# Kernel optimization log

Hardware: AMD Instinct MI355X
Metric: run time of the kernel (lower is better)

The kernel has to match this reference:

```python
import math
import jax, jax.numpy as jnp
import numpy as np

D_MODEL, N_HEADS, QKV, D_HEAD, D_FF, N_BLOCKS, IN_DIM = 288, 8, 328, 41, 1315, 4, 83
B, S = 1024, 128
EPS = 1e-5


def setup_inputs() -> dict:
    key = jax.random.key(0)
    ks = iter(jax.random.split(key, 64))
    def rn(shape, scale=0.05):
        return jax.random.normal(next(ks), shape, jnp.float32) * scale
    inp = {
        "x": jax.random.normal(next(ks), (B, S, IN_DIM), jnp.float32),
        "Wp": rn((D_MODEL, IN_DIM)), "bp": rn((D_MODEL,)),
        "phase": rn((D_MODEL,)),
        "Wq": rn((N_BLOCKS, QKV, D_MODEL)), "bq": rn((N_BLOCKS, QKV)),
        "Wk": rn((N_BLOCKS, QKV, D_MODEL)), "bk": rn((N_BLOCKS, QKV)),
        "Wv": rn((N_BLOCKS, QKV, D_MODEL)), "bv": rn((N_BLOCKS, QKV)),
        "Wo": rn((N_BLOCKS, D_MODEL, QKV)), "bo": rn((N_BLOCKS, D_MODEL)),
        "temp": jnp.ones((N_BLOCKS,), jnp.float32) + rn((N_BLOCKS,), 0.01),
        "qscale": jnp.ones((N_BLOCKS, N_HEADS), jnp.float32) + rn((N_BLOCKS, N_HEADS), 0.01),
        "Wf1": rn((N_BLOCKS, D_FF, D_MODEL)), "bf1": rn((N_BLOCKS, D_FF)),
        "Wf2": rn((N_BLOCKS, D_MODEL, D_FF)), "bf2": rn((N_BLOCKS, D_MODEL)),
        "n1w": jnp.ones((N_BLOCKS, D_MODEL), jnp.float32), "n1b": jnp.zeros((N_BLOCKS, D_MODEL), jnp.float32),
        "n2w": jnp.ones((N_BLOCKS, D_MODEL), jnp.float32), "n2b": jnp.zeros((N_BLOCKS, D_MODEL), jnp.float32),
        "skip": jnp.ones((N_BLOCKS,), jnp.float32),
        "bn_w": jnp.ones((D_MODEL,), jnp.float32), "bn_b": jnp.zeros((D_MODEL,), jnp.float32),
        "bn_mean": rn((D_MODEL,)), "bn_var": jax.random.uniform(next(ks), (D_MODEL,), jnp.float32, 0.5, 1.5),
        "h1w": rn((144, D_MODEL)), "h1b": rn((144,)),
        "h2w": rn((72, 144)), "h2b": rn((72,)),
        "h3w": rn((1, 72)), "h3b": rn((1,)),
        "u1w": rn((72, D_MODEL)), "u1b": rn((72,)),
        "u2w": rn((1, 72)), "u2b": rn((1,)),
    }
    return inp


def _layer_norm(x, w, b):
    mu = jnp.mean(x, axis=-1, keepdims=True)
    var = jnp.mean((x - mu) ** 2, axis=-1, keepdims=True)
    return (x - mu) * jax.lax.rsqrt(var + EPS) * w + b


def reference(x, Wp, bp, phase, Wq, bq, Wk, bk, Wv, bv, Wo, bo, temp, qscale,
              Wf1, bf1, Wf2, bf2, n1w, n1b, n2w, n2b, skip,
              bn_w, bn_b, bn_mean, bn_var,
              h1w, h1b, h2w, h2b, h3w, h3b, u1w, u1b, u2w, u2b):
    Bsz, Sl, _ = x.shape
    # input projection
    h = jnp.einsum('bsi,di->bsd', x, Wp) + bp
    # sinusoidal positional encoding modulated by cos(quantum_phase)
    pos = jnp.arange(Sl, dtype=jnp.float32)[:, None]
    div = jnp.exp(jnp.arange(0, D_MODEL, 2, dtype=jnp.float32) * (-math.log(10000.0) / D_MODEL))
    pe = jnp.zeros((Sl, D_MODEL), jnp.float32)
    pe = pe.at[:, 0::2].set(jnp.sin(pos * div)).at[:, 1::2].set(jnp.cos(pos * div))
    h = h + pe * jnp.cos(phase)

    for l in range(N_BLOCKS):
        # attention with temperature-scaled softmax + post-softmax per-head scale
        q = (jnp.einsum('bsd,qd->bsq', h, Wq[l]) + bq[l]).reshape(Bsz, Sl, N_HEADS, D_HEAD)
        k = (jnp.einsum('bsd,qd->bsq', h, Wk[l]) + bk[l]).reshape(Bsz, Sl, N_HEADS, D_HEAD)
        v = (jnp.einsum('bsd,qd->bsq', h, Wv[l]) + bv[l]).reshape(Bsz, Sl, N_HEADS, D_HEAD)
        scale = math.sqrt(D_HEAD) * temp[l]
        scores = jnp.einsum('bqhd,bkhd->bhqk', q, k) / scale  # [B,H,S,S]
        attn = jax.nn.softmax(scores, axis=-1) * qscale[l][None, :, None, None]
        o = jnp.einsum('bhqk,bkhd->bqhd', attn, v).reshape(Bsz, Sl, QKV)
        o = jnp.einsum('bsq,dq->bsd', o, Wo[l]) + bo[l]
        h = _layer_norm(h + skip[l] * o, n1w[l], n1b[l])
        # GELU FFN (exact erf gelu, dropout inactive in eval)
        f = jax.nn.gelu(jnp.einsum('bsd,fd->bsf', h, Wf1[l]) + bf1[l], approximate=False)
        f = jnp.einsum('bsf,df->bsd', f, Wf2[l]) + bf2[l]
        h = _layer_norm(h + f, n2w[l], n2b[l])

    pooled = jnp.mean(h, axis=1)  # [B, D_MODEL]
    # output head: BatchNorm1d (eval, running stats) -> GELU -> MLP
    z = (pooled - bn_mean) * jax.lax.rsqrt(bn_var + EPS) * bn_w + bn_b
    z = jax.nn.gelu(z, approximate=False)
    z = jax.nn.gelu(z @ h1w.T + h1b, approximate=False)
    z = jax.nn.gelu(z @ h2w.T + h2b, approximate=False)
    pred = z @ h3w.T + h3b  # [B, 1]
    # uncertainty head
    u = jax.nn.relu(pooled @ u1w.T + u1b)
    unc = jax.nn.softplus(u @ u2w.T + u2b)  # [B, 1]
    return pred, unc
```

## Files before the change

kernel.cpp:

```cpp
#include <hip/hip_runtime.h>
#include <cstdint>

typedef __attribute__((ext_vector_type(8))) short short8;
typedef __attribute__((ext_vector_type(4))) short s4v;
typedef __attribute__((ext_vector_type(4))) float floatx4;

#define DEV __device__ __forceinline__

DEV short f2bf(float f) {
  unsigned u = __builtin_bit_cast(unsigned, f);
  u += 0x7fffu + ((u >> 16) & 1u);
  return (short)(u >> 16);
}
DEV short f2bf_ru(float f) {
  unsigned u = __builtin_bit_cast(unsigned, f);
  return (short)((u + 0x8000u) >> 16);
}
DEV float bf2f(short s) {
  unsigned u = ((unsigned)(unsigned short)s) << 16;
  return __builtin_bit_cast(float, u);
}
DEV float gelu_exact(float x) {
  return 0.5f * x * (1.0f + erff(x * 0.70710678118654752f));
}
DEV float gelu_fast(float x) {
  const float t2 = 1.5957691216057308f * (x + 0.044715f * x * x * x);
  return x / (1.0f + __expf(-t2));
}
DEV void gload16(const void* g, void* l) {
  __builtin_amdgcn_global_load_lds((const __attribute__((address_space(1))) void*)g,
                                   (__attribute__((address_space(3))) void*)l,
                                   16, 0, 0);
}

template<int MODE>
__global__ __launch_bounds__(256)
void gemm_kernel(const short* __restrict__ A, const short* __restrict__ Bw,
                 const float* __restrict__ bias, short* __restrict__ C,
                 const float* __restrict__ pe,
                 int K, int lda, int ldb, int ldc, int Nstore, int NT, long hstride)
{
  __shared__ __align__(16) short lds[128 * 136];
  short* Ct = lds;

  const int tid  = threadIdx.x;
  const int wave = tid >> 6, lane = tid & 63;
  const int quad = lane >> 4, r16 = lane & 15;
  const int per = gridDim.x >> 3;
  const int gti = (blockIdx.x & 7) * per + (blockIdx.x >> 3);
  const int mt = gti / NT, nt = gti - mt * NT;
  const int wm = (wave >> 1) * 64, wn = (wave & 1) * 64;

  const long Abase = (long)mt * 128 * lda;
  const long Bbase = (long)nt * 128 * ldb;

  const int row0 = tid >> 2,         cc0 = (tid & 3) ^ ((row0 >> 1) & 3);
  const int row1 = (256 + tid) >> 2, cc1 = ((256 + tid) & 3) ^ ((row1 >> 1) & 3);

  floatx4 acc[4][4] = {};

  auto stage = [&](short* As_, short* Bs_, int k0) {
    gload16(A  + Abase + (long)row0 * lda + k0 + cc0 * 8, &As_[(wave * 64) * 8]);
    gload16(A  + Abase + (long)row1 * lda + k0 + cc1 * 8, &As_[(256 + wave * 64) * 8]);
    gload16(Bw + Bbase + (long)row0 * ldb + k0 + cc0 * 8, &Bs_[(wave * 64) * 8]);
    gload16(Bw + Bbase + (long)row1 * ldb + k0 + cc1 * 8, &Bs_[(256 + wave * 64) * 8]);
  };
  auto compute = [&](const short* As_, const short* Bs_) {
    short8 af[4], bfr[4];
#pragma unroll
    for (int i = 0; i < 4; ++i) {
      const int R = wm + i * 16 + r16;
      af[i] = *(const short8*)&As_[R * 32 + (quad ^ ((R >> 1) & 3)) * 8];
    }
#pragma unroll
    for (int j = 0; j < 4; ++j) {
      const int R = wn + j * 16 + r16;
      bfr[j] = *(const short8*)&Bs_[R * 32 + (quad ^ ((R >> 1) & 3)) * 8];
    }
#pragma unroll
    for (int i = 0; i < 4; ++i)
#pragma unroll
      for (int j = 0; j < 4; ++j)
        acc[i][j] = __builtin_amdgcn_mfma_f32_16x16x32_bf16(bfr[j], af[i], acc[i][j], 0, 0, 0);
  };

  short* const A0  = lds;
  short* const Bb0 = lds + 4096;
  short* const A1  = lds + 8192;
  short* const Bb1 = lds + 12288;

  stage(A0, Bb0, 0);
  __syncthreads();
  int k0 = 0;
  while (true) {
    if (k0 + 32 < K) stage(A1, Bb1, k0 + 32);
    compute(A0, Bb0);
    __syncthreads();
    k0 += 32;
    if (k0 >= K) break;
    if (k0 + 32 < K) stage(A0, Bb0, k0 + 32);
    compute(A1, Bb1);
    __syncthreads();
    k0 += 32;
    if (k0 >= K) break;
  }

  const int mb0 = mt * 128, tb = nt * 128;

#pragma unroll
  for (int j = 0; j < 4; ++j) {
    const int n0 = wn + j * 16 + quad * 4;
    const floatx4 b4 = *(const floatx4*)&bias[tb + n0];
#pragma unroll
    for (int i = 0; i < 4; ++i) {
      const int m = wm + i * 16 + r16;
      floatx4 v = acc[i][j] + b4;
      if (MODE == 1) {
#pragma unroll
        for (int rg = 0; rg < 4; ++rg) v[rg] = gelu_fast(v[rg]);
      }
      if (MODE == 2) {
        const floatx4 p4 = *(const floatx4*)&pe[((mb0 + m) & 127) * 384 + tb + n0];
        v = v + p4;
      }
      s4v o4;
#pragma unroll
      for (int rg = 0; rg < 4; ++rg) o4[rg] = f2bf_ru(v[rg]);
      *(s4v*)&Ct[m * 136 + n0] = o4;
    }
  }
  __syncthreads();

#pragma unroll
  for (int rr = 0; rr < 8; ++rr) {
    const int chunk = rr * 256 + tid;
    const int row = chunk >> 4, ch = chunk & 15;
    const int gcol = tb + ch * 8;
    if (MODE == 3) {
      const int g = gcol / 48, d0 = gcol - g * 48;
      *(short8*)(C + (long)g * hstride + (long)(mb0 + row) * 48 + d0) =
          *(const short8*)&Ct[row * 136 + ch * 8];
    } else if (gcol < Nstore) {
      *(short8*)(C + (long)(mb0 + row) * ldc + gcol) = *(const short8*)&Ct[row * 136 + ch * 8];
    }
  }
}

template<bool AHEAD>
__global__ __launch_bounds__(512, 4)
void gemm_ln_kernel(const short* __restrict__ A, const short* __restrict__ Bw,
                    const float* __restrict__ bias, short* __restrict__ h,
                    const float* __restrict__ lnw, const float* __restrict__ lnb,
                    const float* __restrict__ skip_p, int layer, int use_skip,
                    int K, int lda, int ldb, long ahs)
{
  __shared__ __align__(16) short lds[128 * 296];
  __shared__ float redp[4][2][2][16];
  __shared__ float reds[4][2][2][16];
  short* Hs = lds;

  const int tid  = threadIdx.x;
  const int wave = tid >> 6, lane = tid & 63;
  const int quad = lane >> 4, r16 = lane & 15;
  const int wr = wave >> 1, wc = wave & 1;
  const int mt = blockIdx.x;
  const long mrow0 = (long)mt * 128;

  floatx4 acc[2][9] = {};

  auto stage = [&](short* buf, int k0) {
    for (int c = tid; c < 1664; c += 512) {
      const void* src;
      if (c < 512) {
        const int row = c >> 2, cc = (c & 3) ^ ((row >> 1) & 3);
        if (AHEAD) {
          const int kc = k0 + cc * 8;
          const int g = kc / 48, d = kc - g * 48;
          src = A + (long)g * ahs + (mrow0 + row) * 48 + d;
        } else {
          src = A + (mrow0 + row) * lda + k0 + cc * 8;
        }
      } else {
        const int cb = c - 512;
        const int row = cb >> 2, cc = (cb & 3) ^ ((row >> 1) & 3);
        src = Bw + (long)row * ldb + k0 + cc * 8;
      }
      gload16(src, &buf[(size_t)(c & ~63) * 8]);
    }
  };

  auto compute = [&](const short* buf) {
    const short* As_ = buf;
    const short* Bs_ = buf + 4096;
    const int Ra0 = wr * 32 + r16, Ra1 = Ra0 + 16;
    const short8 af0 = *(const short8*)&As_[Ra0 * 32 + (quad ^ ((Ra0 >> 1) & 3)) * 8];
    const short8 af1 = *(const short8*)&As_[Ra1 * 32 + (quad ^ ((Ra1 >> 1) & 3)) * 8];
#pragma unroll
    for (int t = 0; t < 9; ++t) {
      const int Rb = wc * 144 + t * 16 + r16;
      const short8 b = *(const short8*)&Bs_[Rb * 32 + (quad ^ ((Rb >> 1) & 3)) * 8];
      acc[0][t] = __builtin_amdgcn_mfma_f32_16x16x32_bf16(b, af0, acc[0][t], 0, 0, 0);
      acc[1][t] = __builtin_amdgcn_mfma_f32_16x16x32_bf16(b, af1, acc[1][t], 0, 0, 0);
    }
  };

  short* const B0 = lds;
  short* const B1 = lds + 13312;

  stage(B0, 0);
  __syncthreads();
  int k0 = 0;
  while (true) {
    if (k0 + 32 < K) stage(B1, k0 + 32);
    compute(B0);
    __syncthreads();
    k0 += 32;
    if (k0 >= K) break;
    if (k0 + 32 < K) stage(B0, k0 + 32);
    compute(B1);
    __syncthreads();
    k0 += 32;
    if (k0 >= K) break;
  }

  for (int c = tid; c < 4608; c += 512) {
    const int row = c / 36, ch = c - row * 36;
    *(short8*)&Hs[row * 296 + ch * 8] =
        *(const short8*)(h + (mrow0 + row) * 288 + ch * 8);
  }
  __syncthreads();

  const float skipv = use_skip ? skip_p[layer] : 1.0f;
  const int m0 = wr * 32 + r16, m1 = m0 + 16;

  float ps0 = 0.f, ss0 = 0.f, ps1 = 0.f, ss1 = 0.f;
#pragma unroll
  for (int t = 0; t < 9; ++t) {
    const int n0 = wc * 144 + t * 16 + quad * 4;
    const floatx4 b4 = *(const floatx4*)&bias[n0];
    const s4v h40 = *(const s4v*)&Hs[m0 * 296 + n0];
    const s4v h41 = *(const s4v*)&Hs[m1 * 296 + n0];
#pragma unroll
    for (int rg = 0; rg < 4; ++rg) {
      const float y0 = bf2f(h40[rg]) + skipv * (acc[0][t][rg] + b4[rg]);
      const float y1 = bf2f(h41[rg]) + skipv * (acc[1][t][rg] + b4[rg]);
      acc[0][t][rg] = y0; acc[1][t][rg] = y1;
      ps0 += y0; ss0 += y0 * y0;
      ps1 += y1; ss1 += y1 * y1;
    }
  }
  ps0 += __shfl_xor(ps0, 16); ps0 += __shfl_xor(ps0, 32);
  ss0 += __shfl_xor(ss0, 16); ss0 += __shfl_xor(ss0, 32);
  ps1 += __shfl_xor(ps1, 16); ps1 += __shfl_xor(ps1, 32);
  ss1 += __shfl_xor(ss1, 16); ss1 += __shfl_xor(ss1, 32);
  if (lane < 16) {
    redp[wr][wc][0][r16] = ps0; redp[wr][wc][1][r16] = ps1;
    reds[wr][wc][0][r16] = ss0; reds[wr][wc][1][r16] = ss1;
  }
  __syncthreads();
  const float psum0 = redp[wr][0][0][r16] + redp[wr][1][0][r16];
  const float psum1 = redp[wr][0][1][r16] + redp[wr][1][1][r16];
  const float ssum0 = reds[wr][0][0][r16] + reds[wr][1][0][r16];
  const float ssum1 = reds[wr][0][1][r16] + reds[wr][1][1][r16];
  const float mean0 = psum0 * (1.f / 288.f), mean1 = psum1 * (1.f / 288.f);
  const float rstd0 = rsqrtf(ssum0 * (1.f / 288.f) - mean0 * mean0 + 1e-5f);
  const float rstd1 = rsqrtf(ssum1 * (1.f / 288.f) - mean1 * mean1 + 1e-5f);

#pragma unroll
  for (int t = 0; t < 9; ++t) {
    const int n0 = wc * 144 + t * 16 + quad * 4;
    const floatx4 w4 = *(const floatx4*)&lnw[n0];
    const floatx4 l4 = *(const floatx4*)&lnb[n0];
    s4v o0, o1;
#pragma unroll
    for (int rg = 0; rg < 4; ++rg) {
      o0[rg] = f2bf_ru((acc[0][t][rg] - mean0) * rstd0 * w4[rg] + l4[rg]);
      o1[rg] = f2bf_ru((acc[1][t][rg] - mean1) * rstd1 * w4[rg] + l4[rg]);
    }
    *(s4v*)&Hs[m0 * 296 + n0] = o0;
    *(s4v*)&Hs[m1 * 296 + n0] = o1;
  }
  __syncthreads();

  for (int c = tid; c < 4608; c += 512) {
    const int row = c / 36, ch = c - row * 36;
    *(short8*)(h + (mrow0 + row) * 288 + ch * 8) =
        *(const short8*)&Hs[row * 296 + ch * 8];
  }
}

__global__ __launch_bounds__(256)
void attn_kernel(short* __restrict__ qkv,
                 const float* __restrict__ qscale, int layer, long Mc)
{
  __shared__ __align__(16) short qk[2 * 128 * 72];
  __shared__ __align__(16) short vsT[48 * 136 + 32];
  __shared__ float red[2][2][64];

  short* qs = qk;
  short* ks = qk + 128 * 72;
  short* Pb = qk;

  const int b = blockIdx.x, h = blockIdx.y;
  const int tid = threadIdx.x;
  const long sec = Mc * 48;
  const short* qg = qkv + (long)h * sec + (long)b * 128 * 48;
  const short* kg = qg + 8 * sec;
  const short* vg = qg + 16 * sec;
  short* og = qkv + (long)(16 + h) * sec + (long)b * 128 * 48;

  for (int c = tid; c < 768; c += 256) {
    const int s = c / 6, dc = c - (c / 6) * 6;
    *(short8*)&qs[s * 72 + dc * 8] = *(const short8*)(qg + (long)s * 48 + dc * 8);
    *(short8*)&ks[s * 72 + dc * 8] = *(const short8*)(kg + (long)s * 48 + dc * 8);
  }
  {
    short8 z;
#pragma unroll
    for (int j = 0; j < 8; ++j) z[j] = 0;
    for (int c = tid; c < 384; c += 256) {
      const int s = c / 3, t = c - (c / 3) * 3;
      *(short8*)&qs[s * 72 + 48 + t * 8] = z;
      *(short8*)&ks[s * 72 + 48 + t * 8] = z;
    }
  }
  for (int c = tid; c < 768; c += 256) {
    const int s = c & 127, dc = c >> 7;
    const short8 tv = *(const short8*)(vg + (long)s * 48 + dc * 8);
#pragma unroll
    for (int j = 0; j < 8; ++j) {
      const int row = dc * 8 + j;
      vsT[row * 136 + ((row >> 3) & 3) * 8 + s] = tv[j];
    }
  }
  __syncthreads();

  const int wave = tid >> 6, lane = tid & 63;
  const int quad = lane >> 4, r16 = lane & 15;
  const int wm = (wave >> 1) * 64, wn = (wave & 1) * 64;
  const int rh = wave >> 1, ch = wave & 1;
  const float qsc = qscale[layer * 8 + h];

  floatx4 acc[4][4] = {};
#pragma unroll
  for (int kk = 0; kk < 2; ++kk) {
    const int k0 = kk * 32;
    short8 af[4], bfr[4];
#pragma unroll
    for (int i = 0; i < 4; ++i)
      af[i] = *(const short8*)&qs[(wm + i * 16 + r16) * 72 + k0 + quad * 8];
#pragma unroll
    for (int j = 0; j < 4; ++j)
      bfr[j] = *(const short8*)&ks[(wn + j * 16 + r16) * 72 + k0 + quad * 8];
#pragma unroll
    for (int i = 0; i < 4; ++i)
#pragma unroll
      for (int j = 0; j < 4; ++j)
        acc[i][j] = __builtin_amdgcn_mfma_f32_16x16x32_bf16(bfr[j], af[i], acc[i][j], 0, 0, 0);
  }

  float rmax[4], rsum[4];
#pragma unroll
  for (int i = 0; i < 4; ++i) {
    float m = acc[i][0][0];
#pragma unroll
    for (int j = 0; j < 4; ++j)
#pragma unroll
      for (int rg = 0; rg < 4; ++rg) m = fmaxf(m, acc[i][j][rg]);
    m = fmaxf(m, __shfl_xor(m, 16));
    m = fmaxf(m, __shfl_xor(m, 32));
    rmax[i] = m;
  }
  if (lane < 16)
#pragma unroll
    for (int i = 0; i < 4; ++i) red[rh][ch][i * 16 + r16] = rmax[i];
  __syncthreads();
#pragma unroll
  for (int i = 0; i < 4; ++i)
    rmax[i] = fmaxf(red[rh][0][i * 16 + r16], red[rh][1][i * 16 + r16]);

#pragma unroll
  for (int i = 0; i < 4; ++i) {
    float s = 0.f;
#pragma unroll
    for (int j = 0; j < 4; ++j)
#pragma unroll
      for (int rg = 0; rg < 4; ++rg) {
        const float e = __expf(acc[i][j][rg] - rmax[i]);
        acc[i][j][rg] = e;
        s += e;
      }
    s += __shfl_xor(s, 16);
    s += __shfl_xor(s, 32);
    rsum[i] = s;
  }
  __syncthreads();
  if (lane < 16)
#pragma unroll
    for (int i = 0; i < 4; ++i) red[rh][ch][i * 16 + r16] = rsum[i];
  __syncthreads();
#pragma unroll
  for (int i = 0; i < 4; ++i)
    rmax[i] = qsc / (red[rh][0][i * 16 + r16] + red[rh][1][i * 16 + r16]);

#pragma unroll
  for (int i = 0; i < 4; ++i) {
    const int sq = wm + i * 16 + r16;
#pragma unroll
    for (int j = 0; j < 4; ++j) {
      const int sk0 = wn + j * 16 + quad * 4;
      s4v p4;
#pragma unroll
      for (int rg = 0; rg < 4; ++rg) p4[rg] = f2bf_ru(acc[i][j][rg] * rmax[i]);
      *(s4v*)&Pb[sq * 136 + sk0] = p4;
    }
  }
  __syncthreads();

  const int om = (wave >> 1) * 64, on = (wave & 1) * 32;
  const int jn = (on == 0) ? 2 : 1;
  floatx4 oacc[4][2] = {};
  for (int kk = 0; kk < 4; ++kk) {
    const int k0 = kk * 32;
    short8 af[4], bfr[2];
#pragma unroll
    for (int i = 0; i < 4; ++i)
      af[i] = *(const short8*)&Pb[(om + i * 16 + r16) * 136 + k0 + quad * 8];
    for (int j = 0; j < jn; ++j) {
      const int row = on + j * 16 + r16;
      bfr[j] = *(const short8*)&vsT[row * 136 + ((row >> 3) & 3) * 8 + k0 + quad * 8];
    }
#pragma unroll
    for (int i = 0; i < 4; ++i)
      for (int j = 0; j < jn; ++j)
        oacc[i][j] = __builtin_amdgcn_mfma_f32_16x16x32_bf16(bfr[j], af[i], oacc[i][j], 0, 0, 0);
  }
#pragma unroll
  for (int i = 0; i < 4; ++i)
    for (int j = 0; j < jn; ++j) {
      const int d0 = on + j * 16 + quad * 4;
      const int sq = om + i * 16 + r16;
      s4v o4;
#pragma unroll
      for (int rg = 0; rg < 4; ++rg) o4[rg] = f2bf_ru(oacc[i][j][rg]);
      *(s4v*)(og + (long)sq * 48 + d0) = o4;
    }
}

__global__ __launch_bounds__(256)
void head_kernel(const short* __restrict__ hb, float* __restrict__ out,
                 const float* bn_w, const float* bn_b, const float* bn_mean, const float* bn_var,
                 const float* h1w, const float* h1b, const float* h2w, const float* h2b,
                 const float* h3w, const float* h3b,
                 const float* u1w, const float* u1b, const float* u2w, const float* u2b)
{
  __shared__ float psum[252][8];
  __shared__ float pooled[288], z[288], z1[144], z2[72], uu[72];
  const int b = blockIdx.x, tid = threadIdx.x;

  if (tid < 252) {
    const int cch = tid % 36, grp = tid / 36;
    float a[8];
#pragma unroll
    for (int j = 0; j < 8; ++j) a[j] = 0.f;
    for (int r = grp; r < 128; r += 7) {
      const short8 hv = *(const short8*)(hb + ((long)b * 128 + r) * 288 + cch * 8);
#pragma unroll
      for (int j = 0; j < 8; ++j) a[j] += bf2f(hv[j]);
    }
#pragma unroll
    for (int j = 0; j < 8; ++j) psum[tid][j] = a[j];
  }
  __syncthreads();
  for (int d = tid; d < 288; d += 256) {
    const int cch = d >> 3, j = d & 7;
    float s = 0.f;
#pragma unroll
    for (int g = 0; g < 7; ++g) s += psum[g * 36 + cch][j];
    pooled[d] = s * (1.f / 128.f);
  }
  __syncthreads();

  for (int d = tid; d < 288; d += 256) {
    const float p = pooled[d];
    z[d] = gelu_exact((p - bn_mean[d]) * rsqrtf(bn_var[d] + 1e-5f) * bn_w[d] + bn_b[d]);
  }
  __syncthreads();

  if (tid < 144) {
    float s = h1b[tid];
    for (int k = 0; k < 288; ++k) s += z[k] * h1w[tid * 288 + k];
    z1[tid] = gelu_exact(s);
  } else if (tid < 216) {
    const int t = tid - 144;
    float s = u1b[t];
    for (int k = 0; k < 288; ++k) s += pooled[k] * u1w[t * 288 + k];
    uu[t] = fmaxf(s, 0.f);
  }
  __syncthreads();

  if (tid < 72) {
    float s = h2b[tid];
    for (int k = 0; k < 144; ++k) s += z1[k] * h2w[tid * 144 + k];
    z2[tid] = gelu_exact(s);
  }
  __syncthreads();

  if (tid == 0) {
    float s = h3b[0];
    for (int k = 0; k < 72; ++k) s += z2[k] * h3w[k];
    out[b] = s;
  }
  if (tid == 64) {
    float s = u2b[0];
    for (int k = 0; k < 72; ++k) s += uu[k] * u2w[k];
    out[1024 + b] = (s > 20.f) ? s : log1pf(__expf(s));
  }
}

__global__ void conv_w_kernel(const float* __restrict__ src, short* __restrict__ dst,
                              int N, int K, int Npad, int Kpad, int total)
{
  const int i = blockIdx.x * 256 + threadIdx.x;
  if (i >= total) return;
  const int kk = i % Kpad;
  const int t  = i / Kpad;
  const int n  = t % Npad;
  const int l  = t / Npad;
  const float v = (n < N && kk < K) ? src[((long)l * N + n) * K + kk] : 0.f;
  dst[i] = f2bf(v);
}

__global__ void conv_b_kernel(const float* __restrict__ src, float* __restrict__ dst,
                              int N, int Npad, int total)
{
  const int i = blockIdx.x * 256 + threadIdx.x;
  if (i >= total) return;
  const int n = i % Npad, l = i / Npad;
  dst[i] = (n < N) ? src[l * N + n] : 0.f;
}

__global__ void conv_wqkv_kernel(const float* __restrict__ Wq, const float* __restrict__ Wk,
                                 const float* __restrict__ Wv, const float* __restrict__ temp,
                                 short* __restrict__ dst)
{
  const int i = blockIdx.x * 256 + threadIdx.x;
  if (i >= 4 * 1152 * 288) return;
  const int kk = i % 288;
  const int t  = i / 288;
  const int r  = t % 1152;
  const int l  = t / 1152;
  const int g  = r / 48, d = r - (r / 48) * 48;
  const int sec = g >> 3, head = g & 7;
  float v = 0.f;
  if (d < 41) {
    const float* W = (sec == 0) ? Wq : (sec == 1) ? Wk : Wv;
    v = W[((long)l * 328 + head * 41 + d) * 288 + kk];
    if (sec == 0) v *= 1.0f / (6.4031242374328485f * temp[l]);
  }
  dst[i] = f2bf(v);
}

__global__ void conv_bqkv_kernel(const float* __restrict__ bq, const float* __restrict__ bk,
                                 const float* __restrict__ bv, const float* __restrict__ temp,
                                 float* __restrict__ dst)
{
  const int i = blockIdx.x * 256 + threadIdx.x;
  if (i >= 4 * 1152) return;
  const int r = i % 1152, l = i / 1152;
  const int g = r / 48, d = r - (r / 48) * 48;
  const int sec = g >> 3, head = g & 7;
  float v = 0.f;
  if (d < 41) {
    const float* b = (sec == 0) ? bq : (sec == 1) ? bk : bv;
    v = b[l * 328 + head * 41 + d];
    if (sec == 0) v *= 1.0f / (6.4031242374328485f * temp[l]);
  }
  dst[i] = v;
}

__global__ void conv_wo_kernel(const float* __restrict__ Wo, short* __restrict__ dst)
{
  const int i = blockIdx.x * 256 + threadIdx.x;
  if (i >= 4 * 288 * 384) return;
  const int kk = i % 384;
  const int t  = i / 384;
  const int n  = t % 288;
  const int l  = t / 288;
  const int head = kk / 48, d = kk - head * 48;
  float v = 0.f;
  if (d < 41) v = Wo[((long)l * 288 + n) * 328 + head * 41 + d];
  dst[i] = f2bf(v);
}

__global__ void conv_x_kernel(const float* __restrict__ x, short* __restrict__ xb, int total)
{
  const int i = blockIdx.x * 256 + threadIdx.x;
  if (i >= total) return;
  const int c = i % 96;
  const int r = i / 96;
  xb[i] = f2bf((c < 83) ? x[(long)r * 83 + c] : 0.f);
}

__global__ void pe_kernel(const float* __restrict__ phase, float* __restrict__ pe_mod)
{
  const int i = blockIdx.x * 256 + threadIdx.x;
  if (i >= 128 * 384) return;
  const int d = i % 384, s = i / 384;
  float out = 0.f;
  if (d < 288) {
    const int pair = d >> 1;
    const float divv = expf((float)(2 * pair) * (-9.210340371976184f / 288.f));
    const float arg = (float)s * divv;
    const float v = (d & 1) ? cosf(arg) : sinf(arg);
    out = v * cosf(phase[d]);
  }
  pe_mod[i] = out;
}

extern "C" void kernel_launch(void* const* d_in, const int* in_sizes, int n_in,
                              void* d_out, int out_size, void* d_ws, size_t ws_size,
                              hipStream_t stream)
{
  (void)in_sizes; (void)n_in; (void)out_size;

  const float* x     = (const float*)d_in[0];
  const float* Wp    = (const float*)d_in[1];
  const float* bp    = (const float*)d_in[2];
  const float* phase = (const float*)d_in[3];
  const float* Wq    = (const float*)d_in[4];
  const float* bq    = (const float*)d_in[5];
  const float* Wk    = (const float*)d_in[6];
  const float* bk    = (const float*)d_in[7];
  const float* Wv    = (const float*)d_in[8];
  const float* bv    = (const float*)d_in[9];
  const float* Wo    = (const float*)d_in[10];
  const float* bo    = (const float*)d_in[11];
  const float* temp  = (const float*)d_in[12];
  const float* qscale= (const float*)d_in[13];
  const float* Wf1   = (const float*)d_in[14];
  const float* bf1   = (const float*)d_in[15];
  const float* Wf2   = (const float*)d_in[16];
  const float* bf2   = (const float*)d_in[17];
  const float* n1w   = (const float*)d_in[18];
  const float* n1b   = (const float*)d_in[19];
  const float* n2w   = (const float*)d_in[20];
  const float* n2b   = (const float*)d_in[21];
  const float* skip  = (const float*)d_in[22];
  const float* bn_w  = (const float*)d_in[23];
  const float* bn_b  = (const float*)d_in[24];
  const float* bn_mean=(const float*)d_in[25];
  const float* bn_var= (const float*)d_in[26];
  const float* h1w   = (const float*)d_in[27];
  const float* h1b   = (const float*)d_in[28];
  const float* h2w   = (const float*)d_in[29];
  const float* h2b   = (const float*)d_in[30];
  const float* h3w   = (const float*)d_in[31];
  const float* h3b   = (const float*)d_in[32];
  const float* u1w   = (const float*)d_in[33];
  const float* u1b   = (const float*)d_in[34];
  const float* u2w   = (const float*)d_in[35];
  const float* u2b   = (const float*)d_in[36];

  char* ws = (char*)d_ws;
  size_t off = 0;
  auto alloc = [&](size_t n) -> char* {
    off = (off + 255) & ~(size_t)255;
    char* p = ws + off;
    off += n;
    return p;
  };

  const long M = 131072;

  short* h_bf   = (short*)alloc((size_t)M * 288 * 2);
  float* pe_mod = (float*)alloc(128 * 384 * 4);

  short* Wp_b   = (short*)alloc((size_t)384 * 96 * 2);
  short* Wqkv_b = (short*)alloc((size_t)4 * 1152 * 288 * 2);
  short* Wo_b   = (short*)alloc((size_t)4 * 288 * 384 * 2);
  short* Wf1_b  = (short*)alloc((size_t)4 * 1408 * 288 * 2);
  short* Wf2_b  = (short*)alloc((size_t)4 * 384 * 1344 * 2);

  float* bp_p   = (float*)alloc((size_t)384 * 4);
  float* bqkv_p = (float*)alloc((size_t)4 * 1152 * 4);
  float* bo_p   = (float*)alloc((size_t)4 * 384 * 4);
  float* bf1_p  = (float*)alloc((size_t)4 * 1408 * 4);
  float* bf2_p  = (float*)alloc((size_t)4 * 384 * 4);

  const size_t fixed = off;
  int NC = 1;
  while (NC < 16 && fixed + (size_t)(M / NC) * 2304 + (1u << 20) > ws_size) NC <<= 1;
  const long Mc = M / NC;
  const long Mc2 = Mc / 2;
  const long sec = Mc * 48;

  char* R = alloc((size_t)Mc * 2304);
  short* qkv_bf = (short*)R;
  short* f_bf   = (short*)R;
  short* x_bfc  = (short*)R;

  const dim3 blk(256);

  auto conv_w = [&](const float* s, short* d, int N, int K, int Np, int Kp, int L) {
    const int total = L * Np * Kp;
    conv_w_kernel<<<dim3((total + 255) / 256), blk, 0, stream>>>(s, d, N, K, Np, Kp, total);
  };
  auto conv_b = [&](const float* s, float* d, int N, int Np, int L) {
    const int total = L * Np;
    conv_b_kernel<<<dim3((total + 255) / 256), blk, 0, stream>>>(s, d, N, Np, total);
  };
  conv_w(Wp,  Wp_b,  288,   83, 384,   96, 1);
  conv_wqkv_kernel<<<dim3((4 * 1152 * 288 + 255) / 256), blk, 0, stream>>>(Wq, Wk, Wv, temp, Wqkv_b);
  conv_wo_kernel<<<dim3((4 * 288 * 384 + 255) / 256), blk, 0, stream>>>(Wo, Wo_b);
  conv_w(Wf1, Wf1_b, 1315, 288, 1408, 288, 4);
  conv_w(Wf2, Wf2_b, 288, 1315, 384, 1344, 4);
  conv_b(bp,  bp_p,  288,  384, 1);
  conv_bqkv_kernel<<<dim3((4 * 1152 + 255) / 256), blk, 0, stream>>>(bq, bk, bv, temp, bqkv_p);
  conv_b(bo,  bo_p,  288,  384, 4);
  conv_b(bf1, bf1_p, 1315, 1408, 4);
  conv_b(bf2, bf2_p, 288,  384, 4);
  pe_kernel<<<dim3((128 * 384 + 255) / 256), blk, 0, stream>>>(phase, pe_mod);

  auto gemm = [&](int mode, const short* A, const short* Bmat, const float* bias,
                  short* C, const float* pe, int K, int lda, int ldb, int ldc,
                  int Nstore, int NT, long Mrows, long hstride) {
    const dim3 grid((unsigned)((Mrows / 128) * NT));
    switch (mode) {
      case 0: gemm_kernel<0><<<grid, blk, 0, stream>>>(A, Bmat, bias, C, pe, K, lda, ldb, ldc, Nstore, NT, hstride); break;
      case 1: gemm_kernel<1><<<grid, blk, 0, stream>>>(A, Bmat, bias, C, pe, K, lda, ldb, ldc, Nstore, NT, hstride); break;
      case 2: gemm_kernel<2><<<grid, blk, 0, stream>>>(A, Bmat, bias, C, pe, K, lda, ldb, ldc, Nstore, NT, hstride); break;
      default: gemm_kernel<3><<<grid, blk, 0, stream>>>(A, Bmat, bias, C, pe, K, lda, ldb, ldc, Nstore, NT, hstride); break;
    }
  };

  for (int c = 0; c < NC; ++c) {
    const float* x_c = x + (size_t)c * Mc * 83;
    short* h_c = h_bf + (size_t)c * Mc * 288;

    const int xtot = (int)(Mc * 96);
    conv_x_kernel<<<dim3((xtot + 255) / 256), blk, 0, stream>>>(x_c, x_bfc, xtot);

    gemm(2, x_bfc, Wp_b, bp_p, h_c, pe_mod, 96, 96, 96, 288, 288, 3, Mc, 0);

    for (int l = 0; l < 4; ++l) {
      const short* Wqkv_l = Wqkv_b + (size_t)l * 1152 * 288;
      const short* Wo_l   = Wo_b   + (size_t)l * 288 * 384;
      const short* Wf1_l  = Wf1_b  + (size_t)l * 1408 * 288;
      const short* Wf2_l  = Wf2_b  + (size_t)l * 384 * 1344;

      gemm(3, h_c, Wqkv_l, bqkv_p + l * 1152, qkv_bf, nullptr,
           288, 288, 288, 0, 1152, 9, Mc, sec);

      attn_kernel<<<dim3((unsigned)(Mc / 128), 8), blk, 0, stream>>>(
          qkv_bf, qscale, l, Mc);

      gemm_ln_kernel<true><<<dim3((unsigned)(Mc / 128)), dim3(512), 0, stream>>>(
          qkv_bf + 16 * sec, Wo_l, bo_p + l * 384, h_c, n1w + l * 288, n1b + l * 288,
          skip, l, 1, 384, 48, 384, sec);

      for (int s = 0; s < 2; ++s) {
        short* h_s = h_c + (size_t)s * Mc2 * 288;
        gemm(1, h_s, Wf1_l, bf1_p + l * 1408, f_bf, nullptr,
             288, 288, 288, 1344, 1344, 11, Mc2, 0);
        gemm_ln_kernel<false><<<dim3((unsigned)(Mc2 / 128)), dim3(512), 0, stream>>>(
            f_bf, Wf2_l, bf2_p + l * 384, h_s, n2w + l * 288, n2b + l * 288,
            skip, l, 0, 1344, 1344, 1344, 0);
      }
    }
  }

  head_kernel<<<dim3(1024), blk, 0, stream>>>(h_bf, (float*)d_out,
      bn_w, bn_b, bn_mean, bn_var,
      h1w, h1b, h2w, h2b, h3w, h3b,
      u1w, u1b, u2w, u2b);
}
```

Measured before the change: 3.673 ms.

## Fuse FFN up-projection, GELU, down-projection and LayerNorm into one kernel

Adds an ffn_kernel that keeps the 128-row h tile in registers, computes each 128-column chunk of the FF1 output with GELU into LDS, and immediately accumulates it into the FF2 output. The residual add and LayerNorm are applied at the end, so the large intermediate activation never goes to global memory and two launches per half-chunk are removed. Wf2 padding changes to a 1408 stride to match the chunking. The generic GEMM also loses its LDS double buffering in favour of a single buffer with two barriers per k-step, which can expose load latency in the QKV and input-projection GEMMs.

```diff
diff --git a/kernel.cpp b/kernel.cpp
--- a/kernel.cpp
+++ b/kernel.cpp
@@ -41,6 +41,8 @@
                  int K, int lda, int ldb, int ldc, int Nstore, int NT, long hstride)
 {
   __shared__ __align__(16) short lds[128 * 136];
+  short* As = lds;
+  short* Bs = lds + 128 * 32;
   short* Ct = lds;
 
   const int tid  = threadIdx.x;
@@ -59,54 +61,35 @@
 
   floatx4 acc[4][4] = {};
 
-  auto stage = [&](short* As_, short* Bs_, int k0) {
-    gload16(A  + Abase + (long)row0 * lda + k0 + cc0 * 8, &As_[(wave * 64) * 8]);
-    gload16(A  + Abase + (long)row1 * lda + k0 + cc1 * 8, &As_[(256 + wave * 64) * 8]);
-    gload16(Bw + Bbase + (long)row0 * ldb + k0 + cc0 * 8, &Bs_[(wave * 64) * 8]);
-    gload16(Bw + Bbase + (long)row1 * ldb + k0 + cc1 * 8, &Bs_[(256 + wave * 64) * 8]);
-  };
-  auto compute = [&](const short* As_, const short* Bs_) {
+  for (int k0 = 0; k0 < K; k0 += 32) {
+    __syncthreads();
+    gload16(A  + Abase + (long)row0 * lda + k0 + cc0 * 8, &As[(0 * 256 + wave * 64) * 8]);
+    gload16(A  + Abase + (long)row1 * lda + k0 + cc1 * 8, &As[(1 * 256 + wave * 64) * 8]);
+    gload16(Bw + Bbase + (long)row0 * ldb + k0 + cc0 * 8, &Bs[(0 * 256 + wave * 64) * 8]);
+    gload16(Bw + Bbase + (long)row1 * ldb + k0 + cc1 * 8, &Bs[(1 * 256 + wave * 64) * 8]);
+    __syncthreads();
+
     short8 af[4], bfr[4];
 #pragma unroll
     for (int i = 0; i < 4; ++i) {
       const int R = wm + i * 16 + r16;
-      af[i] = *(const short8*)&As_[R * 32 + (quad ^ ((R >> 1) & 3)) * 8];
+      af[i] = *(const short8*)&As[R * 32 + (quad ^ ((R >> 1) & 3)) * 8];
     }
 #pragma unroll
     for (int j = 0; j < 4; ++j) {
       const int R = wn + j * 16 + r16;
-      bfr[j] = *(const short8*)&Bs_[R * 32 + (quad ^ ((R >> 1) & 3)) * 8];
+      bfr[j] = *(const short8*)&Bs[R * 32 + (quad ^ ((R >> 1) & 3)) * 8];
     }
 #pragma unroll
     for (int i = 0; i < 4; ++i)
 #pragma unroll
       for (int j = 0; j < 4; ++j)
         acc[i][j] = __builtin_amdgcn_mfma_f32_16x16x32_bf16(bfr[j], af[i], acc[i][j], 0, 0, 0);
-  };
-
-  short* const A0  = lds;
-  short* const Bb0 = lds + 4096;
-  short* const A1  = lds + 8192;
-  short* const Bb1 = lds + 12288;
-
-  stage(A0, Bb0, 0);
-  __syncthreads();
-  int k0 = 0;
-  while (true) {
-    if (k0 + 32 < K) stage(A1, Bb1, k0 + 32);
-    compute(A0, Bb0);
-    __syncthreads();
-    k0 += 32;
-    if (k0 >= K) break;
-    if (k0 + 32 < K) stage(A0, Bb0, k0 + 32);
-    compute(A1, Bb1);
-    __syncthreads();
-    k0 += 32;
-    if (k0 >= K) break;
   }
 
   const int mb0 = mt * 128, tb = nt * 128;
 
+  __syncthreads();
 #pragma unroll
   for (int j = 0; j < 4; ++j) {
     const int n0 = wn + j * 16 + quad * 4;
@@ -286,6 +269,189 @@
     const int row = c / 36, ch = c - row * 36;
     *(short8*)(h + (mrow0 + row) * 288 + ch * 8) =
         *(const short8*)&Hs[row * 296 + ch * 8];
+  }
+}
+
+__global__ __launch_bounds__(512, 2)
+void ffn_kernel(short* __restrict__ h,
+                const short* __restrict__ W1, const float* __restrict__ b1,
+                const short* __restrict__ W2, const float* __restrict__ b2,
+                const float* __restrict__ lnw, const float* __restrict__ lnb)
+{
+  __shared__ __align__(16) short lds[128 * 296];
+  __shared__ float redp[4][2][2][16];
+  __shared__ float reds[4][2][2][16];
+  short* const fl = lds + 18432;
+
+  const int tid  = threadIdx.x;
+  const int wave = tid >> 6, lane = tid & 63;
+  const int quad = lane >> 4, r16 = lane & 15;
+  const int wr = wave >> 1, wp = wave & 1;
+  const long mrow0 = (long)blockIdx.x * 128;
+
+  short8 ha[2][9];
+#pragma unroll
+  for (int i = 0; i < 2; ++i) {
+    const long rb = (mrow0 + wr * 32 + i * 16 + r16) * 288L;
+#pragma unroll
+    for (int k9 = 0; k9 < 9; ++k9)
+      ha[i][k9] = *(const short8*)(h + rb + k9 * 32 + quad * 8);
+  }
+
+  floatx4 acc2[2][9] = {};
+
+  const int srow = tid >> 2, scc = (tid & 3) ^ ((srow >> 1) & 3);
+
+  auto stageW1 = [&](int c, int k9, short* dst) {
+    gload16(W1 + ((long)(c * 128 + srow)) * 288 + k9 * 32 + scc * 8,
+            &dst[(size_t)(tid & ~63) * 8]);
+  };
+  auto stageW2 = [&](int c, int ks, short* dst) {
+    for (int c2 = tid; c2 < 1152; c2 += 512) {
+      const int row = c2 >> 2, cc = (c2 & 3) ^ ((row >> 1) & 3);
+      gload16(W2 + (long)row * 1408 + c * 128 + ks * 32 + cc * 8,
+              &dst[(size_t)(c2 & ~63) * 8]);
+    }
+  };
+
+  stageW1(0, 0, lds);
+  __syncthreads();
+  int cur = 0;
+
+  for (int c = 0; c < 11; ++c) {
+    floatx4 acc1[2][4] = {};
+
+#pragma unroll
+    for (int k9 = 0; k9 < 9; ++k9) {
+      short* const Sn = lds + (cur ^ 1) * 9216;
+      if (k9 < 8) stageW1(c, k9 + 1, Sn);
+      else        stageW2(c, 0, Sn);
+
+      const short* Sc = lds + cur * 9216;
+      short8 bfr[4];
+#pragma unroll
+      for (int j = 0; j < 4; ++j) {
+        const int R = wp * 64 + j * 16 + r16;
+        bfr[j] = *(const short8*)&Sc[R * 32 + (quad ^ ((R >> 1) & 3)) * 8];
+      }
+#pragma unroll
+      for (int i = 0; i < 2; ++i)
+#pragma unroll
+        for (int j = 0; j < 4; ++j)
+          acc1[i][j] = __builtin_amdgcn_mfma_f32_16x16x32_bf16(bfr[j], ha[i][k9], acc1[i][j], 0, 0, 0);
+
+      if (k9 == 8) {
+#pragma unroll
+        for (int i = 0; i < 2; ++i) {
+          const int m = wr * 32 + i * 16 + r16;
+#pragma unroll
+          for (int j = 0; j < 4; ++j) {
+            const int nb = c * 128 + wp * 64 + j * 16 + quad * 4;
+            const floatx4 b4 = *(const floatx4*)&b1[nb];
+            s4v o;
+#pragma unroll
+            for (int rg = 0; rg < 4; ++rg)
+              o[rg] = f2bf_ru(gelu_fast(acc1[i][j][rg] + b4[rg]));
+            const int ks = wp * 2 + (j >> 1);
+            const int mg = ((j & 1) * 2 + (quad >> 1)) ^ ((m >> 1) & 3);
+            *(s4v*)&fl[ks * 4096 + m * 32 + mg * 8 + (quad & 1) * 4] = o;
+          }
+        }
+      }
+      __syncthreads();
+      cur ^= 1;
+    }
+
+#pragma unroll
+    for (int ks = 0; ks < 4; ++ks) {
+      short* const Sn = lds + (cur ^ 1) * 9216;
+      if (ks < 3)      stageW2(c, ks + 1, Sn);
+      else if (c < 10) stageW1(c + 1, 0, Sn);
+
+      const short* Sc = lds + cur * 9216;
+      short8 af2[2], br[9];
+#pragma unroll
+      for (int i = 0; i < 2; ++i) {
+        const int R = wr * 32 + i * 16 + r16;
+        af2[i] = *(const short8*)&fl[ks * 4096 + R * 32 + (quad ^ ((R >> 1) & 3)) * 8];
+      }
+#pragma unroll
+      for (int t = 0; t < 9; ++t) {
+        const int R = wp * 144 + t * 16 + r16;
+        br[t] = *(const short8*)&Sc[R * 32 + (quad ^ ((R >> 1) & 3)) * 8];
+      }
+#pragma unroll
+      for (int i = 0; i < 2; ++i)
+#pragma unroll
+        for (int t = 0; t < 9; ++t)
+          acc2[i][t] = __builtin_amdgcn_mfma_f32_16x16x32_bf16(br[t], af2[i], acc2[i][t], 0, 0, 0);
+
+      __syncthreads();
+      cur ^= 1;
+    }
+  }
+
+  for (int c2 = tid; c2 < 4608; c2 += 512) {
+    const int row = c2 / 36, ch = c2 - row * 36;
+    *(short8*)&lds[row * 296 + ch * 8] =
+        *(const short8*)(h + (mrow0 + row) * 288 + ch * 8);
+  }
+  __syncthreads();
+
+  const int m0 = wr * 32 + r16, m1 = m0 + 16;
+  float ps0 = 0.f, ss0 = 0.f, ps1 = 0.f, ss1 = 0.f;
+#pragma unroll
+  for (int t = 0; t < 9; ++t) {
+    const int n0 = wp * 144 + t * 16 + quad * 4;
+    const floatx4 b4 = *(const floatx4*)&b2[n0];
+    const s4v h40 = *(const s4v*)&lds[m0 * 296 + n0];
+    const s4v h41 = *(const s4v*)&lds[m1 * 296 + n0];
+#pragma unroll
+    for (int rg = 0; rg < 4; ++rg) {
+      const float y0 = bf2f(h40[rg]) + acc2[0][t][rg] + b4[rg];
+      const float y1 = bf2f(h41[rg]) + acc2[1][t][rg] + b4[rg];
+      acc2[0][t][rg] = y0; acc2[1][t][rg] = y1;
+      ps0 += y0; ss0 += y0 * y0;
+      ps1 += y1; ss1 += y1 * y1;
+    }
+  }
+  ps0 += __shfl_xor(ps0, 16); ps0 += __shfl_xor(ps0, 32);
+  ss0 += __shfl_xor(ss0, 16); ss0 += __shfl_xor(ss0, 32);
+  ps1 += __shfl_xor(ps1, 16); ps1 += __shfl_xor(ps1, 32);
+  ss1 += __shfl_xor(ss1, 16); ss1 += __shfl_xor(ss1, 32);
+  if (lane < 16) {
+    redp[wr][wp][0][r16] = ps0; redp[wr][wp][1][r16] = ps1;
+    reds[wr][wp][0][r16] = ss0; reds[wr][wp][1][r16] = ss1;
+  }
+  __syncthreads();
+  const float psum0 = redp[wr][0][0][r16] + redp[wr][1][0][r16];
+  const float psum1 = redp[wr][0][1][r16] + redp[wr][1][1][r16];
+  const float ssum0 = reds[wr][0][0][r16] + reds[wr][1][0][r16];
+  const float ssum1 = reds[wr][0][1][r16] + reds[wr][1][1][r16];
+  const float mean0 = psum0 * (1.f / 288.f), mean1 = psum1 * (1.f / 288.f);
+  const float rstd0 = rsqrtf(ssum0 * (1.f / 288.f) - mean0 * mean0 + 1e-5f);
+  const float rstd1 = rsqrtf(ssum1 * (1.f / 288.f) - mean1 * mean1 + 1e-5f);
+
+#pragma unroll
+  for (int t = 0; t < 9; ++t) {
+    const int n0 = wp * 144 + t * 16 + quad * 4;
+    const floatx4 w4 = *(const floatx4*)&lnw[n0];
+    const floatx4 l4 = *(const floatx4*)&lnb[n0];
+    s4v o0, o1;
+#pragma unroll
+    for (int rg = 0; rg < 4; ++rg) {
+      o0[rg] = f2bf_ru((acc2[0][t][rg] - mean0) * rstd0 * w4[rg] + l4[rg]);
+      o1[rg] = f2bf_ru((acc2[1][t][rg] - mean1) * rstd1 * w4[rg] + l4[rg]);
+    }
+    *(s4v*)&lds[m0 * 296 + n0] = o0;
+    *(s4v*)&lds[m1 * 296 + n0] = o1;
+  }
+  __syncthreads();
+
+  for (int c2 = tid; c2 < 4608; c2 += 512) {
+    const int row = c2 / 36, ch = c2 - row * 36;
+    *(short8*)(h + (mrow0 + row) * 288 + ch * 8) =
+        *(const short8*)&lds[row * 296 + ch * 8];
   }
 }
 
@@ -680,7 +846,7 @@
   short* Wqkv_b = (short*)alloc((size_t)4 * 1152 * 288 * 2);
   short* Wo_b   = (short*)alloc((size_t)4 * 288 * 384 * 2);
   short* Wf1_b  = (short*)alloc((size_t)4 * 1408 * 288 * 2);
-  short* Wf2_b  = (short*)alloc((size_t)4 * 384 * 1344 * 2);
+  short* Wf2_b  = (short*)alloc((size_t)4 * 384 * 1408 * 2);
 
   float* bp_p   = (float*)alloc((size_t)384 * 4);
   float* bqkv_p = (float*)alloc((size_t)4 * 1152 * 4);
@@ -692,12 +858,10 @@
   int NC = 1;
   while (NC < 16 && fixed + (size_t)(M / NC) * 2304 + (1u << 20) > ws_size) NC <<= 1;
   const long Mc = M / NC;
-  const long Mc2 = Mc / 2;
   const long sec = Mc * 48;
 
   char* R = alloc((size_t)Mc * 2304);
   short* qkv_bf = (short*)R;
-  short* f_bf   = (short*)R;
   short* x_bfc  = (short*)R;
 
   const dim3 blk(256);
@@ -714,7 +878,7 @@
   conv_wqkv_kernel<<<dim3((4 * 1152 * 288 + 255) / 256), blk, 0, stream>>>(Wq, Wk, Wv, temp, Wqkv_b);
   conv_wo_kernel<<<dim3((4 * 288 * 384 + 255) / 256), blk, 0, stream>>>(Wo, Wo_b);
   conv_w(Wf1, Wf1_b, 1315, 288, 1408, 288, 4);
-  conv_w(Wf2, Wf2_b, 288, 1315, 384, 1344, 4);
+  conv_w(Wf2, Wf2_b, 288, 1315, 384, 1408, 4);
   conv_b(bp,  bp_p,  288,  384, 1);
   conv_bqkv_kernel<<<dim3((4 * 1152 + 255) / 256), blk, 0, stream>>>(bq, bk, bv, temp, bqkv_p);
   conv_b(bo,  bo_p,  288,  384, 4);
@@ -747,7 +911,7 @@
       const short* Wqkv_l = Wqkv_b + (size_t)l * 1152 * 288;
       const short* Wo_l   = Wo_b   + (size_t)l * 288 * 384;
       const short* Wf1_l  = Wf1_b  + (size_t)l * 1408 * 288;
-      const short* Wf2_l  = Wf2_b  + (size_t)l * 384 * 1344;
+      const short* Wf2_l  = Wf2_b  + (size_t)l * 384 * 1408;
 
       gemm(3, h_c, Wqkv_l, bqkv_p + l * 1152, qkv_bf, nullptr,
            288, 288, 288, 0, 1152, 9, Mc, sec);
@@ -759,14 +923,9 @@
           qkv_bf + 16 * sec, Wo_l, bo_p + l * 384, h_c, n1w + l * 288, n1b + l * 288,
           skip, l, 1, 384, 48, 384, sec);
 
-      for (int s = 0; s < 2; ++s) {
-        short* h_s = h_c + (size_t)s * Mc2 * 288;
-        gemm(1, h_s, Wf1_l, bf1_p + l * 1408, f_bf, nullptr,
-             288, 288, 288, 1344, 1344, 11, Mc2, 0);
-        gemm_ln_kernel<false><<<dim3((unsigned)(Mc2 / 128)), dim3(512), 0, stream>>>(
-            f_bf, Wf2_l, bf2_p + l * 384, h_s, n2w + l * 288, n2b + l * 288,
-            skip, l, 0, 1344, 1344, 1344, 0);
-      }
+      ffn_kernel<<<dim3((unsigned)(Mc / 128)), dim3(512), 0, stream>>>(
+          h_c, Wf1_l, bf1_p + l * 1408, Wf2_l, bf2_p + l * 384,
+          n2w + l * 288, n2b + l * 288);
     }
   }
 
```

Result: faster. 3.492 ms (-4.9%).
